# Kernel tuning notes

Hardware: AMD Instinct MI355X
Metric: run time of the kernel (lower is better)

The kernel has to match this reference:

```python
import jax, jax.numpy as jnp
import numpy as np

B, N_IN, N_HID, N_OUT = 4096, 1024, 4096, 1024

def setup_inputs() -> dict:
    key = jax.random.key(0)
    k_x, k_w1, k_b1, k_w2, k_b2 = jax.random.split(key, 5)
    # Per-node LiveNet weights, batched: each hidden neuron = relu(sum_i w_i * in_i + b),
    # each output neuron = linear sum over hidden neurons.
    s1 = 1.0 / np.sqrt(N_IN)
    s2 = 1.0 / np.sqrt(N_HID)
    return {
        "x": jax.random.normal(k_x, (B, N_IN), dtype=jnp.float32),
        "W1": jax.random.uniform(k_w1, (N_IN, N_HID), jnp.float32, -s1, s1),
        "b1": jax.random.uniform(k_b1, (N_HID,), jnp.float32, -s1, s1),
        "W2": jax.random.uniform(k_w2, (N_HID, N_OUT), jnp.float32, -s2, s2),
        "b2": jax.random.uniform(k_b2, (N_OUT,), jnp.float32, -s2, s2),
    }

def reference(x, W1, b1, W2, b2):
    # Batched equivalent of LiveNet's per-node traversal:
    # inputs[i].set_output(x[:, i:i+1]); each hidden neuron computes
    # relu(weighted sum of parents + bias); each output node is a linear
    # weighted sum of hidden outputs; outputs concatenated along dim=1.
    h = jax.nn.relu(x @ W1 + b1)          # [B, N_HID]
    y = h @ W2 + b2                        # [B, N_OUT]
    return y
```

## Files before the change

kernel.cpp:

```cpp
#include <hip/hip_runtime.h>
#include <stdint.h>

#define BDIM  4096
#define NIN   1024
#define NHID  4096
#define NOUT  1024

typedef unsigned short u16;
typedef unsigned int   u32;
typedef __attribute__((ext_vector_type(8))) __bf16 bf16x8;
typedef __attribute__((ext_vector_type(4))) float  f32x4;

__device__ __forceinline__ u16 f32_to_bf16_rne(float f) {
    u32 u = __builtin_bit_cast(u32, f);
    u = (u + 0x7fffu + ((u >> 16) & 1u)) >> 16;
    return (u16)u;
}

__device__ __forceinline__ void transpose_tile(
    const float* __restrict__ in, u16* __restrict__ out,
    int R, int C, int bx, int by, float (*tile)[33]) {
    const int rt = by * 32, ct = bx * 32;
    const int tid = threadIdx.x;
    {
        const int r  = tid >> 3;
        const int c4 = (tid & 7) * 4;
        float4 v = *(const float4*)(in + (size_t)(rt + r) * C + ct + c4);
        tile[r][c4 + 0] = v.x; tile[r][c4 + 1] = v.y;
        tile[r][c4 + 2] = v.z; tile[r][c4 + 3] = v.w;
    }
    __syncthreads();
    if (tid < 128) {
        const int oc = tid >> 2;
        const int ch = tid & 3;
        u16 tmp[8];
#pragma unroll
        for (int j = 0; j < 8; ++j)
            tmp[j] = f32_to_bf16_rne(tile[ch * 8 + j][oc]);
        u16* dst = out + (size_t)(ct + oc) * R + rt + ch * 8;
        ushort4 lo = {tmp[0], tmp[1], tmp[2], tmp[3]};
        ushort4 hi = {tmp[4], tmp[5], tmp[6], tmp[7]};
        *(ushort4*)dst = lo;
        *(ushort4*)(dst + 4) = hi;
    }
}

__global__ void prepass(const float* __restrict__ x,  u16* __restrict__ x_bf,
                        const float* __restrict__ W1, u16* __restrict__ W1t,
                        const float* __restrict__ W2, u16* __restrict__ W2t) {
    __shared__ float tile[32][33];
    const int b = blockIdx.x;
    if (b < 4096) {
        int i = b * 256 + threadIdx.x;
        float4 v = ((const float4*)x)[i];
        ushort4 o;
        o.x = f32_to_bf16_rne(v.x); o.y = f32_to_bf16_rne(v.y);
        o.z = f32_to_bf16_rne(v.z); o.w = f32_to_bf16_rne(v.w);
        ((ushort4*)x_bf)[i] = o;
    } else if (b < 8192) {
        int t = b - 4096;
        transpose_tile(W1, W1t, NIN, NHID, t & 127, t >> 7, tile);
    } else {
        int t = b - 8192;
        transpose_tile(W2, W2t, NHID, NOUT, t & 31, t >> 5, tile);
    }
}

__global__ __launch_bounds__(256) void gemm_bt_relu(
    const u16* __restrict__ A, const u16* __restrict__ Bt,
    const float* __restrict__ bias, u16* __restrict__ outp,
    int M, int N, int K)
{
    constexpr int MI = 4, NI = 4;
    __shared__ __align__(16) u16 smemA[128 * 64];
    __shared__ __align__(16) u16 smemB[128 * 64];

    const int tid  = threadIdx.x;
    const int lane = tid & 63;
    const int wave = tid >> 6;
    const int rowBase = blockIdx.y * 128;
    const int colBase = blockIdx.x * 128;
    const int wrow = (wave >> 1) * 64;
    const int wcol = (wave & 1) * 64;

    f32x4 acc[MI][NI] = {};

    const int srow    = lane >> 3;
    const int chunkSw = (lane & 7) ^ srow;
    const int gcol    = chunkSw * 8;
    const int fr = lane & 15;
    const int fq = lane >> 4;
    const int sw = fr & 7;

    for (int k0 = 0; k0 < K; k0 += 64) {
        __syncthreads();
#pragma unroll
        for (int t = 0; t < 4; ++t) {
            int region = wave * 4 + t;
            int arow = rowBase + region * 8 + srow;
            const u16* g = A + (size_t)arow * K + k0 + gcol;
            __builtin_amdgcn_global_load_lds(
                (const __attribute__((address_space(1))) u32*)g,
                (__attribute__((address_space(3))) u32*)(smemA + region * 512),
                16, 0, 0);
        }
#pragma unroll
        for (int t = 0; t < 4; ++t) {
            int region = wave * 4 + t;
            int brow = colBase + region * 8 + srow;
            const u16* g = Bt + (size_t)brow * K + k0 + gcol;
            __builtin_amdgcn_global_load_lds(
                (const __attribute__((address_space(1))) u32*)g,
                (__attribute__((address_space(3))) u32*)(smemB + region * 512),
                16, 0, 0);
        }
        __builtin_amdgcn_s_waitcnt(0);
        __syncthreads();

#pragma unroll
        for (int s = 0; s < 2; ++s) {
            const int co = ((s * 4 + fq) ^ sw) * 16;
            const char* aB = (const char*)smemA + (wrow + fr) * 128 + co;
            const char* bB = (const char*)smemB + (wcol + fr) * 128 + co;
            bf16x8 af[MI], bfv[NI];
#pragma unroll
            for (int mi = 0; mi < MI; ++mi)
                af[mi] = *(const bf16x8*)(aB + mi * 2048);
#pragma unroll
            for (int ni = 0; ni < NI; ++ni)
                bfv[ni] = *(const bf16x8*)(bB + ni * 2048);
#pragma unroll
            for (int mi = 0; mi < MI; ++mi)
#pragma unroll
                for (int ni = 0; ni < NI; ++ni)
                    acc[mi][ni] = __builtin_amdgcn_mfma_f32_16x16x32_bf16(
                        af[mi], bfv[ni], acc[mi][ni], 0, 0, 0);
        }
    }

    const int col0 = colBase + wcol + fr;
    const int row0 = rowBase + wrow + (fq << 2);
#pragma unroll
    for (int ni = 0; ni < NI; ++ni) {
        const int col = col0 + ni * 16;
        const float bv = bias[col];
#pragma unroll
        for (int mi = 0; mi < MI; ++mi) {
            const int row = row0 + mi * 16;
#pragma unroll
            for (int r = 0; r < 4; ++r) {
                float v = acc[mi][ni][r] + bv;
                v = v > 0.f ? v : 0.f;
                outp[(size_t)(row + r) * N + col] = f32_to_bf16_rne(v);
            }
        }
    }
}

__global__ __launch_bounds__(256) void gemm2_splitk(
    const u16* __restrict__ A, const u16* __restrict__ Bt,
    const float* __restrict__ bias, float* __restrict__ out0,
    int M, int N, int K, int Kchunk)
{
    constexpr int MI = 4, NI = 4;
    __shared__ __align__(16) u16 smemA[128 * 64];
    __shared__ __align__(16) u16 smemB[128 * 64];

    const int tid  = threadIdx.x;
    const int lane = tid & 63;
    const int wave = tid >> 6;
    const int rowBase = blockIdx.y * 128;
    const int colBase = blockIdx.x * 128;
    const int z    = blockIdx.z;
    const int kBeg = z * Kchunk;
    const int kEnd = kBeg + Kchunk;
    const int wrow = (wave >> 1) * 64;
    const int wcol = (wave & 1) * 64;

    f32x4 acc[MI][NI] = {};

    const int srow    = lane >> 3;
    const int chunkSw = (lane & 7) ^ srow;
    const int gcol    = chunkSw * 8;
    const int fr = lane & 15;
    const int fq = lane >> 4;
    const int sw = fr & 7;

    for (int k0 = kBeg; k0 < kEnd; k0 += 64) {
        __syncthreads();
#pragma unroll
        for (int t = 0; t < 4; ++t) {
            int region = wave * 4 + t;
            int arow = rowBase + region * 8 + srow;
            const u16* g = A + (size_t)arow * K + k0 + gcol;
            __builtin_amdgcn_global_load_lds(
                (const __attribute__((address_space(1))) u32*)g,
                (__attribute__((address_space(3))) u32*)(smemA + region * 512),
                16, 0, 0);
        }
#pragma unroll
        for (int t = 0; t < 4; ++t) {
            int region = wave * 4 + t;
            int brow = colBase + region * 8 + srow;
            const u16* g = Bt + (size_t)brow * K + k0 + gcol;
            __builtin_amdgcn_global_load_lds(
                (const __attribute__((address_space(1))) u32*)g,
                (__attribute__((address_space(3))) u32*)(smemB + region * 512),
                16, 0, 0);
        }
        __builtin_amdgcn_s_waitcnt(0);
        __syncthreads();

#pragma unroll
        for (int s = 0; s < 2; ++s) {
            const int co = ((s * 4 + fq) ^ sw) * 16;
            const char* aB = (const char*)smemA + (wrow + fr) * 128 + co;
            const char* bB = (const char*)smemB + (wcol + fr) * 128 + co;
            bf16x8 af[MI], bfv[NI];
#pragma unroll
            for (int mi = 0; mi < MI; ++mi)
                af[mi] = *(const bf16x8*)(aB + mi * 2048);
#pragma unroll
            for (int ni = 0; ni < NI; ++ni)
                bfv[ni] = *(const bf16x8*)(bB + ni * 2048);
#pragma unroll
            for (int mi = 0; mi < MI; ++mi)
#pragma unroll
                for (int ni = 0; ni < NI; ++ni)
                    acc[mi][ni] = __builtin_amdgcn_mfma_f32_16x16x32_bf16(
                        af[mi], bfv[ni], acc[mi][ni], 0, 0, 0);
        }
    }

    const int col0 = colBase + wcol + fr;
    const int row0 = rowBase + wrow + (fq << 2);
#pragma unroll
    for (int ni = 0; ni < NI; ++ni) {
        const int col = col0 + ni * 16;
        const float bv = (z == 0) ? bias[col] : 0.f;
#pragma unroll
        for (int mi = 0; mi < MI; ++mi) {
            const int row = row0 + mi * 16;
#pragma unroll
            for (int r = 0; r < 4; ++r)
                atomicAdd(&out0[(size_t)(row + r) * N + col],
                          acc[mi][ni][r] + bv);
        }
    }
}

extern "C" void kernel_launch(void* const* d_in, const int* in_sizes, int n_in,
                              void* d_out, int out_size, void* d_ws, size_t ws_size,
                              hipStream_t stream) {
    const float* x  = (const float*)d_in[0];
    const float* W1 = (const float*)d_in[1];
    const float* b1 = (const float*)d_in[2];
    const float* W2 = (const float*)d_in[3];
    const float* b2 = (const float*)d_in[4];

    char* ws = (char*)d_ws;
    const size_t MB = 1024 * 1024;
    u16* W2t  = (u16*)(ws + 0 * MB);
    u16* h_bf = (u16*)(ws + 8 * MB);
    u16* x_bf = (u16*)(ws + 40 * MB);
    u16* W1t  = (u16*)(ws + 48 * MB);

    hipMemsetAsync(d_out, 0, (size_t)BDIM * NOUT * sizeof(float), stream);

    prepass<<<12288, 256, 0, stream>>>(x, x_bf, W1, W1t, W2, W2t);

    gemm_bt_relu<<<dim3(NHID / 128, BDIM / 128), 256, 0, stream>>>(
        x_bf, W1t, b1, h_bf, BDIM, NHID, NIN);

    gemm2_splitk<<<dim3(NOUT / 128, BDIM / 128, 2), 256, 0, stream>>>(
        h_bf, W2t, b2, (float*)d_out, BDIM, NOUT, NHID, NHID / 2);
}
```

Baseline: 209.4 us.

## Remap GEMM blocks per XCD for L2 locality and replace split-K atomics with reduce

Both GEMMs now launch on a 1D grid and remap the block id so that blocks landing on the same XCD (bid & 7) cover a compact 2D patch of output tiles, which is meant to improve L2 reuse of A and B tiles. The second GEMM drops its fp32 atomicAdd split-K epilogue and the memset. The two K-halves are written to d_out and to a workspace buffer, and a separate elementwise kernel adds them together with the bias. This removes atomic traffic and the memset at the cost of an extra launch and an extra read and write of a 16MB partial buffer.

Result: faster. 192.0 us (-8.3%).

```diff
diff --git a/kernel.cpp b/kernel.cpp
--- a/kernel.cpp
+++ b/kernel.cpp
@@ -75,11 +75,17 @@
     __shared__ __align__(16) u16 smemA[128 * 64];
     __shared__ __align__(16) u16 smemB[128 * 64];
 
+    const int bid = blockIdx.x;
+    const int cxcd = bid & 7;
+    const int j    = bid >> 3;
+    const int bx   = ((cxcd & 3) << 3) + (j & 7);
+    const int by   = ((cxcd >> 2) << 4) + (j >> 3);
+
     const int tid  = threadIdx.x;
     const int lane = tid & 63;
     const int wave = tid >> 6;
-    const int rowBase = blockIdx.y * 128;
-    const int colBase = blockIdx.x * 128;
+    const int rowBase = by * 128;
+    const int colBase = bx * 128;
     const int wrow = (wave >> 1) * 64;
     const int wcol = (wave & 1) * 64;
 
@@ -159,19 +165,25 @@
 
 __global__ __launch_bounds__(256) void gemm2_splitk(
     const u16* __restrict__ A, const u16* __restrict__ Bt,
-    const float* __restrict__ bias, float* __restrict__ out0,
+    float* __restrict__ out0, float* __restrict__ p1,
     int M, int N, int K, int Kchunk)
 {
     constexpr int MI = 4, NI = 4;
     __shared__ __align__(16) u16 smemA[128 * 64];
     __shared__ __align__(16) u16 smemB[128 * 64];
 
+    const int bid = blockIdx.x;
+    const int cxcd = bid & 7;
+    const int j    = bid >> 3;
+    const int z    = cxcd >> 2;
+    const int bx   = j & 7;
+    const int by   = ((cxcd & 3) << 3) + (j >> 3);
+
     const int tid  = threadIdx.x;
     const int lane = tid & 63;
     const int wave = tid >> 6;
-    const int rowBase = blockIdx.y * 128;
-    const int colBase = blockIdx.x * 128;
-    const int z    = blockIdx.z;
+    const int rowBase = by * 128;
+    const int colBase = bx * 128;
     const int kBeg = z * Kchunk;
     const int kEnd = kBeg + Kchunk;
     const int wrow = (wave >> 1) * 64;
@@ -232,21 +244,34 @@
         }
     }
 
+    float* outp = (z == 0) ? out0 : p1;
     const int col0 = colBase + wcol + fr;
     const int row0 = rowBase + wrow + (fq << 2);
 #pragma unroll
     for (int ni = 0; ni < NI; ++ni) {
         const int col = col0 + ni * 16;
-        const float bv = (z == 0) ? bias[col] : 0.f;
 #pragma unroll
         for (int mi = 0; mi < MI; ++mi) {
             const int row = row0 + mi * 16;
 #pragma unroll
             for (int r = 0; r < 4; ++r)
-                atomicAdd(&out0[(size_t)(row + r) * N + col],
-                          acc[mi][ni][r] + bv);
-        }
-    }
+                outp[(size_t)(row + r) * N + col] = acc[mi][ni][r];
+        }
+    }
+}
+
+__global__ void splitk_reduce(float* __restrict__ out0,
+                              const float* __restrict__ p,
+                              const float* __restrict__ bias,
+                              int n4, int nCols4) {
+    int i = blockIdx.x * blockDim.x + threadIdx.x;
+    if (i >= n4) return;
+    float4 v = ((const float4*)out0)[i];
+    float4 q = ((const float4*)p)[i];
+    float4 bv = ((const float4*)bias)[i & (nCols4 - 1)];
+    v.x += q.x + bv.x; v.y += q.y + bv.y;
+    v.z += q.z + bv.z; v.w += q.w + bv.w;
+    ((float4*)out0)[i] = v;
 }
 
 extern "C" void kernel_launch(void* const* d_in, const int* in_sizes, int n_in,
@@ -260,18 +285,21 @@
 
     char* ws = (char*)d_ws;
     const size_t MB = 1024 * 1024;
-    u16* W2t  = (u16*)(ws + 0 * MB);
-    u16* h_bf = (u16*)(ws + 8 * MB);
-    u16* x_bf = (u16*)(ws + 40 * MB);
-    u16* W1t  = (u16*)(ws + 48 * MB);
-
-    hipMemsetAsync(d_out, 0, (size_t)BDIM * NOUT * sizeof(float), stream);
+    u16*   W2t  = (u16*)(ws + 0 * MB);
+    u16*   h_bf = (u16*)(ws + 8 * MB);
+    u16*   x_bf = (u16*)(ws + 40 * MB);
+    u16*   W1t  = (u16*)(ws + 48 * MB);
+    float* p1   = (float*)(ws + 56 * MB);
 
     prepass<<<12288, 256, 0, stream>>>(x, x_bf, W1, W1t, W2, W2t);
 
-    gemm_bt_relu<<<dim3(NHID / 128, BDIM / 128), 256, 0, stream>>>(
+    gemm_bt_relu<<<1024, 256, 0, stream>>>(
         x_bf, W1t, b1, h_bf, BDIM, NHID, NIN);
 
-    gemm2_splitk<<<dim3(NOUT / 128, BDIM / 128, 2), 256, 0, stream>>>(
-        h_bf, W2t, b2, (float*)d_out, BDIM, NOUT, NHID, NHID / 2);
-}
+    gemm2_splitk<<<512, 256, 0, stream>>>(
+        h_bf, W2t, (float*)d_out, p1, BDIM, NOUT, NHID, NHID / 2);
+
+    int rn4 = BDIM * NOUT / 4;
+    splitk_reduce<<<(rn4 + 255) / 256, 256, 0, stream>>>(
+        (float*)d_out, p1, b2, rn4, NOUT / 4);
+}
```

## Replace atomic split-K with intra-block K split and remap blocks per XCD

Applied to the files above, without the earlier changes.

The second GEMM now splits K across two groups of four waves inside one 512-thread block. The halves are combined through shared memory, and the result is written with plain stores instead of global float atomics, which also removes the output memset. Both GEMMs use a 1D grid whose block indices are remapped so blocks landing on the same XCD share nearby A and B tiles for better L2 reuse. The cost is fewer, larger blocks for GEMM2 (256 blocks of 512 threads) and 64KB of LDS per block, which may reduce occupancy.

Measured after the change: 194.6 us. -7.1%, faster.

```diff
diff --git a/kernel.cpp b/kernel.cpp
--- a/kernel.cpp
+++ b/kernel.cpp
@@ -75,11 +75,17 @@
     __shared__ __align__(16) u16 smemA[128 * 64];
     __shared__ __align__(16) u16 smemB[128 * 64];
 
+    const int bid = blockIdx.x;
+    const int cxcd = bid & 7;
+    const int j    = bid >> 3;
+    const int bx   = ((cxcd & 3) << 3) + (j & 7);
+    const int by   = ((cxcd >> 2) << 4) + (j >> 3);
+
     const int tid  = threadIdx.x;
     const int lane = tid & 63;
     const int wave = tid >> 6;
-    const int rowBase = blockIdx.y * 128;
-    const int colBase = blockIdx.x * 128;
+    const int rowBase = by * 128;
+    const int colBase = bx * 128;
     const int wrow = (wave >> 1) * 64;
     const int wcol = (wave & 1) * 64;
 
@@ -157,25 +163,36 @@
     }
 }
 
-__global__ __launch_bounds__(256) void gemm2_splitk(
+__global__ __launch_bounds__(512) void gemm2_fused(
     const u16* __restrict__ A, const u16* __restrict__ Bt,
-    const float* __restrict__ bias, float* __restrict__ out0,
-    int M, int N, int K, int Kchunk)
+    const float* __restrict__ bias, float* __restrict__ outp,
+    int M, int N, int K)
 {
     constexpr int MI = 4, NI = 4;
-    __shared__ __align__(16) u16 smemA[128 * 64];
-    __shared__ __align__(16) u16 smemB[128 * 64];
+    __shared__ __align__(16) u16 smem[4][8192];
+    float* combine = (float*)smem;
+
+    const int bid = blockIdx.x;
+    const int cxcd = bid & 7;
+    const int j    = bid >> 3;
+    const int by   = (cxcd << 2) + (j & 3);
+    const int bx   = j >> 2;
 
     const int tid  = threadIdx.x;
     const int lane = tid & 63;
     const int wave = tid >> 6;
-    const int rowBase = blockIdx.y * 128;
-    const int colBase = blockIdx.x * 128;
-    const int z    = blockIdx.z;
-    const int kBeg = z * Kchunk;
-    const int kEnd = kBeg + Kchunk;
-    const int wrow = (wave >> 1) * 64;
-    const int wcol = (wave & 1) * 64;
+    const int half = wave >> 2;
+    const int w    = wave & 3;
+    const int rowBase = by * 128;
+    const int colBase = bx * 128;
+    const int Kh   = K >> 1;
+    const int kBeg = half * Kh;
+    const int kEnd = kBeg + Kh;
+    const int wrow = (w >> 1) * 64;
+    const int wcol = (w & 1) * 64;
+
+    u16* smA = smem[2 * half];
+    u16* smB = smem[2 * half + 1];
 
     f32x4 acc[MI][NI] = {};
 
@@ -190,22 +207,22 @@
         __syncthreads();
 #pragma unroll
         for (int t = 0; t < 4; ++t) {
-            int region = wave * 4 + t;
+            int region = w * 4 + t;
             int arow = rowBase + region * 8 + srow;
             const u16* g = A + (size_t)arow * K + k0 + gcol;
             __builtin_amdgcn_global_load_lds(
                 (const __attribute__((address_space(1))) u32*)g,
-                (__attribute__((address_space(3))) u32*)(smemA + region * 512),
+                (__attribute__((address_space(3))) u32*)(smA + region * 512),
                 16, 0, 0);
         }
 #pragma unroll
         for (int t = 0; t < 4; ++t) {
-            int region = wave * 4 + t;
+            int region = w * 4 + t;
             int brow = colBase + region * 8 + srow;
             const u16* g = Bt + (size_t)brow * K + k0 + gcol;
             __builtin_amdgcn_global_load_lds(
                 (const __attribute__((address_space(1))) u32*)g,
-                (__attribute__((address_space(3))) u32*)(smemB + region * 512),
+                (__attribute__((address_space(3))) u32*)(smB + region * 512),
                 16, 0, 0);
         }
         __builtin_amdgcn_s_waitcnt(0);
@@ -214,8 +231,8 @@
 #pragma unroll
         for (int s = 0; s < 2; ++s) {
             const int co = ((s * 4 + fq) ^ sw) * 16;
-            const char* aB = (const char*)smemA + (wrow + fr) * 128 + co;
-            const char* bB = (const char*)smemB + (wcol + fr) * 128 + co;
+            const char* aB = (const char*)smA + (wrow + fr) * 128 + co;
+            const char* bB = (const char*)smB + (wcol + fr) * 128 + co;
             bf16x8 af[MI], bfv[NI];
 #pragma unroll
             for (int mi = 0; mi < MI; ++mi)
@@ -232,19 +249,33 @@
         }
     }
 
-    const int col0 = colBase + wcol + fr;
-    const int row0 = rowBase + wrow + (fq << 2);
-#pragma unroll
-    for (int ni = 0; ni < NI; ++ni) {
-        const int col = col0 + ni * 16;
-        const float bv = (z == 0) ? bias[col] : 0.f;
-#pragma unroll
-        for (int mi = 0; mi < MI; ++mi) {
-            const int row = row0 + mi * 16;
-#pragma unroll
-            for (int r = 0; r < 4; ++r)
-                atomicAdd(&out0[(size_t)(row + r) * N + col],
-                          acc[mi][ni][r] + bv);
+    const int lcol0 = wcol + fr;
+    const int lrow0 = wrow + (fq << 2);
+    __syncthreads();
+    if (half == 1) {
+#pragma unroll
+        for (int ni = 0; ni < NI; ++ni)
+#pragma unroll
+            for (int mi = 0; mi < MI; ++mi)
+                *(f32x4*)(combine + (lcol0 + ni * 16) * 128 + lrow0 + mi * 16)
+                    = acc[mi][ni];
+    }
+    __syncthreads();
+    if (half == 0) {
+#pragma unroll
+        for (int ni = 0; ni < NI; ++ni) {
+            const int col = colBase + lcol0 + ni * 16;
+            const float bv = bias[col];
+#pragma unroll
+            for (int mi = 0; mi < MI; ++mi) {
+                const int row = rowBase + lrow0 + mi * 16;
+                f32x4 q = *(const f32x4*)(combine +
+                    (lcol0 + ni * 16) * 128 + lrow0 + mi * 16);
+#pragma unroll
+                for (int r = 0; r < 4; ++r)
+                    outp[(size_t)(row + r) * N + col]
+                        = acc[mi][ni][r] + q[r] + bv;
+            }
         }
     }
 }
@@ -265,13 +296,11 @@
     u16* x_bf = (u16*)(ws + 40 * MB);
     u16* W1t  = (u16*)(ws + 48 * MB);
 
-    hipMemsetAsync(d_out, 0, (size_t)BDIM * NOUT * sizeof(float), stream);
-
     prepass<<<12288, 256, 0, stream>>>(x, x_bf, W1, W1t, W2, W2t);
 
-    gemm_bt_relu<<<dim3(NHID / 128, BDIM / 128), 256, 0, stream>>>(
+    gemm_bt_relu<<<1024, 256, 0, stream>>>(
         x_bf, W1t, b1, h_bf, BDIM, NHID, NIN);
 
-    gemm2_splitk<<<dim3(NOUT / 128, BDIM / 128, 2), 256, 0, stream>>>(
-        h_bf, W2t, b2, (float*)d_out, BDIM, NOUT, NHID, NHID / 2);
-}
+    gemm2_fused<<<256, 512, 0, stream>>>(
+        h_bf, W2t, b2, (float*)d_out, BDIM, NOUT, NHID);
+}
```
